# Performance work log

Measured on AMD Instinct MI355X. Metric: run time of the kernel, lower is better.

The kernel has to match this reference:

```python
import jax, jax.numpy as jnp
import numpy as np
from jax import lax

RES = 32          # feature map side, HW = RES*RES = 1024
HEADS = 32
QKD = 16          # sampled_qkdim
VD = 32           # sampled_vdim
L = HEADS * VD    # 1024, v channels

def _relative_position_index(res):
    # faithful to attn_pos_idx in the torch code
    coords = np.stack(np.meshgrid(np.arange(res), np.arange(res), indexing='ij'))  # [2,res,res]
    flat = coords.reshape(2, -1)
    rel = flat[:, :, None] - flat[:, None, :]        # [2, N, N]
    rel = rel.transpose(1, 2, 0).copy()
    rel[:, :, 0] += res - 1
    rel[:, :, 1] += res - 1
    rel[:, :, 0] *= 2 * res - 1
    return rel.sum(-1)                               # [N, N] int

_RPI = jnp.asarray(_relative_position_index(RES))    # [1024,1024]

def _hardswish(x):
    return x * jnp.clip(x + 3.0, 0.0, 6.0) * (1.0 / 6.0)

def setup_inputs() -> dict:
    key = jax.random.key(0)
    ks = jax.random.split(key, 6)
    B, HW, C = 4, RES * RES, 512
    x = jax.random.normal(ks[0], (B, HW, C), jnp.float32)
    w_qkv = jax.random.normal(ks[1], (2 * C + L, C), jnp.float32) * 0.02   # [2048,512]
    dw_kernel = jax.random.normal(ks[2], (L, 1, 3, 3), jnp.float32) * 0.1  # depthwise OIHW
    attn_bias = jax.random.normal(ks[3], ((2 * RES - 1) ** 2, HEADS), jnp.float32) * 0.02
    proj_w = jax.random.normal(ks[4], (C, L), jnp.float32) * 0.02
    proj_b = jax.random.normal(ks[5], (C,), jnp.float32) * 0.02
    return {"x": x, "w_qkv": w_qkv, "dw_kernel": dw_kernel,
            "attn_bias": attn_bias, "proj_w": proj_w, "proj_b": proj_b}

def reference(x, w_qkv, dw_kernel, attn_bias, proj_w, proj_b):
    B, HW, C = x.shape
    # elastic QKV projection (full sampled config == full weight)
    qkv = jnp.einsum('bnc,oc->bno', x, w_qkv)                    # [B,HW,2048]
    qkv = qkv.reshape(B, HW, HEADS, QKD + QKD + VD)
    q, k, v = jnp.split(qkv, [QKD, 2 * QKD], axis=3)             # per-head split
    q = q.transpose(0, 2, 1, 3)                                  # [B,H,HW,qkd]
    k = k.transpose(0, 2, 1, 3)
    # depthwise 3x3 conv on V path
    vimg = v.reshape(B, HW, L).transpose(0, 2, 1).reshape(B, L, RES, RES)
    vimg = lax.conv_general_dilated(vimg, dw_kernel, (1, 1), 'SAME',
                                    feature_group_count=L,
                                    dimension_numbers=('NCHW', 'OIHW', 'NCHW'))
    v = vimg.reshape(B, L, HW).transpose(0, 2, 1).reshape(B, HW, HEADS, VD)
    v = v.transpose(0, 2, 1, 3)                                  # [B,H,HW,vd]
    # attention with relative position bias
    attn = jnp.einsum('bhqd,bhkd->bhqk', q, k) * (QKD ** -0.5)   # [B,H,HW,HW]
    bias = attn_bias[_RPI.reshape(-1)].reshape(HW, HW, HEADS)
    bias = bias.transpose(2, 0, 1)[None]                         # [1,H,HW,HW]
    attn = jax.nn.softmax(attn + bias, axis=-1)
    out = jnp.einsum('bhqk,bhkd->bhqd', attn, v)
    out = out.transpose(0, 2, 1, 3).reshape(B, HW, L)
    out = _hardswish(out)
    out = jnp.einsum('bnl,cl->bnc', out, proj_w) + proj_b
    return out
```

## Files before the change

### kernel.cpp

```cpp
#include <hip/hip_runtime.h>
#include <stdint.h>

#define HEADS 32
#define HW_N 1024
#define QS 0.36067376022224085f
#define LOG2E 1.4426950408889634f

typedef __attribute__((ext_vector_type(8))) __bf16 bf16x8;
typedef __attribute__((ext_vector_type(4))) float f32x4;
typedef __attribute__((ext_vector_type(16))) float f32x16;
typedef __attribute__((ext_vector_type(4))) uint32_t u32x4;

__device__ __forceinline__ float b2f(uint16_t u) {
  union { uint32_t i; float f; } v; v.i = ((uint32_t)u) << 16; return v.f;
}
__device__ __forceinline__ uint16_t f2b(float f) {
  uint32_t u = __builtin_bit_cast(uint32_t, f);
  return (uint16_t)((u + 0x7FFFu + ((u >> 16) & 1u)) >> 16);
}

#define GLD16(g, s) __builtin_amdgcn_global_load_lds( \
    (const __attribute__((address_space(1))) void*)(g), \
    (__attribute__((address_space(3))) void*)(s), 16, 0, 0)

__global__ __launch_bounds__(256) void prep(const float* __restrict__ x,
                                            const float* __restrict__ wqv,
                                            const float* __restrict__ pw,
                                            const float* __restrict__ abias,
                                            uint16_t* __restrict__ xb,
                                            uint16_t* __restrict__ wqb,
                                            uint16_t* __restrict__ pwb,
                                            uint16_t* __restrict__ bt2b) {
  const int blk = blockIdx.x;
  const int tid = threadIdx.x;
  if (blk < 3584) {
    const float* in; uint16_t* out; int i;
    if (blk < 2048)      { in = x;   out = xb;  i = blk * 256 + tid; }
    else if (blk < 3072) { in = wqv; out = wqb; i = (blk - 2048) * 256 + tid; }
    else                 { in = pw;  out = pwb; i = (blk - 3072) * 256 + tid; }
    float4 v = ((const float4*)in)[i];
    ushort4 o;
    o.x = f2b(v.x); o.y = f2b(v.y); o.z = f2b(v.z); o.w = f2b(v.w);
    ((ushort4*)out)[i] = o;
  } else {
    const int blk2 = blk - 3584;
    const int h = blk2 / 63, d31 = blk2 - h * 63;
    const size_t tb = ((size_t)(h * 63 + d31)) << 10;
#pragma unroll
    for (int c = 0; c < 4; ++c) {
      const int idx = c * 256 + tid;
      const int lane = idx >> 4, r = idx & 15;
      const int hi = lane >> 5, ln = lane & 31;
      const int crow = (r & 3) + 8 * (r >> 2) + 4 * hi;
      const int col = 31 + ln - crow;
      bt2b[tb + idx] = f2b(LOG2E * abias[(size_t)(d31 * 63 + col) * 32 + h]);
    }
  }
}

__global__ __launch_bounds__(256) void gemm_qkv(
    const uint16_t* __restrict__ Aop, const uint16_t* __restrict__ Bop,
    uint16_t* __restrict__ qT, uint16_t* __restrict__ ko, uint16_t* __restrict__ vo) {
  const int K = 512;
  __shared__ uint16_t As[2][128 * 32];
  __shared__ uint16_t Bs[2][128 * 32];
  const int tid = threadIdx.x;
  const int lane = tid & 63;
  const int wave = tid >> 6;
  const int am0 = blockIdx.y * 128;
  const int bn0 = blockIdx.x * 128;
  const int m_off = (wave >> 1) * 64;
  const int n_off = (wave & 1) * 64;
  const int sr = tid >> 2;
  const int sc = (tid & 3) << 3;

  auto stage = [&](int buf, int kt) {
    const int k0 = kt << 5;
    GLD16(Aop + (size_t)(am0 + sr) * K + (k0 + sc), &As[buf][tid * 8]);
    GLD16(Aop + (size_t)(am0 + sr + 64) * K + (k0 + sc), &As[buf][(tid + 256) * 8]);
    GLD16(Bop + (size_t)(bn0 + sr) * K + (k0 + sc), &Bs[buf][tid * 8]);
    GLD16(Bop + (size_t)(bn0 + sr + 64) * K + (k0 + sc), &Bs[buf][(tid + 256) * 8]);
  };

  f32x4 acc[4][4] = {};
  stage(0, 0);
  asm volatile("s_waitcnt vmcnt(0)" ::: "memory");
  __syncthreads();

  const int fr = lane & 15;
  const int fk = (lane >> 4) << 3;
  int cur = 0;
  for (int kt = 0; kt < 16; ++kt) {
    if (kt + 1 < 16) stage(cur ^ 1, kt + 1);
    bf16x8 af[4], bf_[4];
#pragma unroll
    for (int mi = 0; mi < 4; ++mi)
      af[mi] = *(const bf16x8*)&As[cur][(m_off + mi * 16 + fr) * 32 + fk];
#pragma unroll
    for (int ni = 0; ni < 4; ++ni)
      bf_[ni] = *(const bf16x8*)&Bs[cur][(n_off + ni * 16 + fr) * 32 + fk];
#pragma unroll
    for (int mi = 0; mi < 4; ++mi)
#pragma unroll
      for (int ni = 0; ni < 4; ++ni)
        acc[mi][ni] = __builtin_amdgcn_mfma_f32_16x16x32_bf16(af[mi], bf_[ni], acc[mi][ni], 0, 0, 0);
    asm volatile("s_waitcnt vmcnt(0)" ::: "memory");
    __syncthreads();
    cur ^= 1;
  }

  const int rb = (lane >> 4) << 2;
  const int cl = lane & 15;
  const int b = am0 >> 10;
  const int h = (bn0 + n_off) >> 6;
  const int bh = b * 32 + h;
#pragma unroll
  for (int mi = 0; mi < 4; ++mi) {
    const int n0 = (am0 & 1023) + m_off + mi * 16 + rb;
    {
      ushort4 o;
      o.x = f2b(acc[mi][0][0] * QS); o.y = f2b(acc[mi][0][1] * QS);
      o.z = f2b(acc[mi][0][2] * QS); o.w = f2b(acc[mi][0][3] * QS);
      *(ushort4*)&qT[((size_t)(bh * 16 + cl) << 10) + n0] = o;
    }
#pragma unroll
    for (int r = 0; r < 4; ++r)
      ko[((size_t)(bh * 1024 + n0 + r)) * 16 + cl] = f2b(acc[mi][1][r]);
#pragma unroll
    for (int nv = 2; nv < 4; ++nv) {
      const int l = h * 32 + (nv - 2) * 16 + cl;
      ushort4 o;
      o.x = f2b(acc[mi][nv][0]); o.y = f2b(acc[mi][nv][1]);
      o.z = f2b(acc[mi][nv][2]); o.w = f2b(acc[mi][nv][3]);
      *(ushort4*)&vo[((size_t)(b * 1024 + l) << 10) + n0] = o;
    }
  }
}

__global__ __launch_bounds__(256) void dwconv3x3(const uint16_t* __restrict__ vimg,
                                                 const float* __restrict__ kw,
                                                 uint16_t* __restrict__ vcv) {
  __shared__ float t[1024];
  const int bl = blockIdx.x;
  const int l = bl & 1023;
  const int tid = threadIdx.x;
  const uint16_t* src = vimg + (size_t)bl * 1024;
  {
    uint2 vv = ((const uint2*)src)[tid];
    t[tid * 4 + 0] = b2f((uint16_t)vv.x);
    t[tid * 4 + 1] = b2f((uint16_t)(vv.x >> 16));
    t[tid * 4 + 2] = b2f((uint16_t)vv.y);
    t[tid * 4 + 3] = b2f((uint16_t)(vv.y >> 16));
  }
  float w[9];
#pragma unroll
  for (int i = 0; i < 9; ++i) w[i] = kw[l * 9 + i];
  __syncthreads();
  uint16_t* dst = vcv + (size_t)bl * 1024;
#pragma unroll
  for (int i = 0; i < 4; ++i) {
    const int p = tid + i * 256;
    const int y = p >> 5, x = p & 31;
    float a = 0.f;
#pragma unroll
    for (int dy = 0; dy < 3; ++dy) {
      const int yy = y + dy - 1;
      if (yy < 0 || yy > 31) continue;
#pragma unroll
      for (int dx = 0; dx < 3; ++dx) {
        const int xx = x + dx - 1;
        if (xx < 0 || xx > 31) continue;
        a += t[yy * 32 + xx] * w[dy * 3 + dx];
      }
    }
    dst[p] = f2b(a);
  }
}

__global__ __launch_bounds__(256, 4) void attn_mfma(
    const uint16_t* __restrict__ qT, const uint16_t* __restrict__ kb,
    const uint16_t* __restrict__ vt, const uint16_t* __restrict__ bt2b,
    uint16_t* __restrict__ hsO) {
  __shared__ __align__(16) uint16_t Ks[2][2][512];
  __shared__ __align__(16) uint16_t Vs[2][2][1024];
  __shared__ __align__(16) uint16_t Bs[7 * 1024];
  __shared__ float inv_s[128];
  const int blk = blockIdx.x;
  const int bh = blk & 127;
  const int qtg = blk >> 7;
  const int b = bh >> 5, h = bh & 31;
  const int tid = threadIdx.x;
  const int wave = tid >> 6, lane = tid & 63;
  const int hi = lane >> 5, ln = lane & 31;

  const int q0 = qtg * 128 + wave * 32;
  const int qi0 = qtg * 4;
  const int qi = qi0 + wave;

  union { ushort u[8]; bf16x8 v; } qu;
#pragma unroll
  for (int j = 0; j < 8; ++j)
    qu.u[j] = qT[((size_t)(bh * 16 + hi * 8 + j) << 10) + q0 + ln];
  const bf16x8 qf = qu.v;

  auto stageKV = [&](int buf, int t2) {
    if (tid < 128) {
      const int tile = tid >> 6, j = tid & 63;
      GLD16(kb + ((size_t)bh * 1024 + (t2 + tile) * 32 + (j & 31)) * 16 + ((j >> 5) & 1) * 8,
            &Ks[buf][tile][j * 8]);
    }
    {
      const int tile = tid >> 7, j = tid & 127;
      GLD16(vt + (((size_t)b * 1024 + h * 32 + (j & 31)) << 10) + (t2 + tile) * 32 + ((j >> 5) & 1) * 8 + ((j >> 6) & 1) * 16,
            &Vs[buf][tile][j * 8]);
    }
  };
  auto stageB = [&](int d31, int half) {
    if ((tid >> 7) == half) {
      const int j = tid & 127;
      GLD16(bt2b + (((size_t)h * 63 + d31) << 10) + (j & 63) * 16 + ((j >> 6) & 1) * 8,
            &Bs[(d31 % 7) * 1024 + j * 8]);
    }
  };

  stageKV(0, 0);
  stageB(qi0 + 30, 0); stageB(qi0 + 31, 1);
  stageB(qi0 + 32, 0); stageB(qi0 + 33, 1);
  stageB(qi0 + 34, 0);
  __syncthreads();

  f32x16 oacc = {};
  float ls0 = 0.f, ls1 = 0.f;
  int cur = 0;
  int slotA = (qi + 31) % 7;

#define COMPUTE(kf, ca, cb, vf0, vf1) do {                            \
    f32x16 cc;                                                        \
    _Pragma("unroll")                                                 \
    for (int j = 0; j < 4; ++j) {                                     \
      const uint32_t ua = ca[j], ub = cb[j];                          \
      cc[2 * j]     = __builtin_bit_cast(float, ua << 16);            \
      cc[2 * j + 1] = __builtin_bit_cast(float, ua & 0xFFFF0000u);    \
      cc[8 + 2 * j]     = __builtin_bit_cast(float, ub << 16);        \
      cc[8 + 2 * j + 1] = __builtin_bit_cast(float, ub & 0xFFFF0000u);\
    }                                                                 \
    const f32x16 s = __builtin_amdgcn_mfma_f32_32x32x16_bf16(kf, qf, cc, 0, 0, 0); \
    float p[16];                                                      \
    _Pragma("unroll")                                                 \
    for (int r = 0; r < 16; ++r) p[r] = __builtin_amdgcn_exp2f(s[r]); \
    _Pragma("unroll")                                                 \
    for (int r = 0; r < 8; ++r) { ls0 += p[r]; ls1 += p[r + 8]; }     \
    uint32_t w0, w1, w2, w3, w4, w5, w6, w7;                          \
    w0 = __builtin_amdgcn_perm(__builtin_bit_cast(uint32_t, p[1]),  __builtin_bit_cast(uint32_t, p[0]),  0x07060302u); \
    w1 = __builtin_amdgcn_perm(__builtin_bit_cast(uint32_t, p[3]),  __builtin_bit_cast(uint32_t, p[2]),  0x07060302u); \
    w2 = __builtin_amdgcn_perm(__builtin_bit_cast(uint32_t, p[5]),  __builtin_bit_cast(uint32_t, p[4]),  0x07060302u); \
    w3 = __builtin_amdgcn_perm(__builtin_bit_cast(uint32_t, p[7]),  __builtin_bit_cast(uint32_t, p[6]),  0x07060302u); \
    w4 = __builtin_amdgcn_perm(__builtin_bit_cast(uint32_t, p[9]),  __builtin_bit_cast(uint32_t, p[8]),  0x07060302u); \
    w5 = __builtin_amdgcn_perm(__builtin_bit_cast(uint32_t, p[11]), __builtin_bit_cast(uint32_t, p[10]), 0x07060302u); \
    w6 = __builtin_amdgcn_perm(__builtin_bit_cast(uint32_t, p[13]), __builtin_bit_cast(uint32_t, p[12]), 0x07060302u); \
    w7 = __builtin_amdgcn_perm(__builtin_bit_cast(uint32_t, p[15]), __builtin_bit_cast(uint32_t, p[14]), 0x07060302u); \
    asm("v_permlane32_swap_b32 %0, %1" : "+v"(w0), "+v"(w2));         \
    asm("v_permlane32_swap_b32 %0, %1" : "+v"(w1), "+v"(w3));         \
    asm("v_permlane32_swap_b32 %0, %1" : "+v"(w4), "+v"(w6));         \
    asm("v_permlane32_swap_b32 %0, %1" : "+v"(w5), "+v"(w7));         \
    const u32x4 a0u = {w0, w1, w2, w3};                               \
    const u32x4 a1u = {w4, w5, w6, w7};                               \
    oacc = __builtin_amdgcn_mfma_f32_32x32x16_bf16(                   \
        __builtin_bit_cast(bf16x8, a0u), vf0, oacc, 0, 0, 0);         \
    oacc = __builtin_amdgcn_mfma_f32_32x32x16_bf16(                   \
        __builtin_bit_cast(bf16x8, a1u), vf1, oacc, 0, 0, 0);         \
  } while (0)

  for (int s = 0; s < 16; ++s) {
    if (s < 15) {
      stageKV(cur ^ 1, 2 * s + 2);
      stageB(qi0 + 29 - 2 * s, 0);
      stageB(qi0 + 28 - 2 * s, 1);
    }
    const int slotB = slotA ? slotA - 1 : 6;
    {
      const bf16x8 kf  = *(const bf16x8*)&Ks[cur][0][lane * 8];
      const bf16x8 vf0 = *(const bf16x8*)&Vs[cur][0][lane * 8];
      const bf16x8 vf1 = *(const bf16x8*)&Vs[cur][0][512 + lane * 8];
      const u32x4 ca = *(const u32x4*)&Bs[slotA * 1024 + lane * 8];
      const u32x4 cb = *(const u32x4*)&Bs[slotA * 1024 + 512 + lane * 8];
      COMPUTE(kf, ca, cb, vf0, vf1);
    }
    {
      const bf16x8 kf  = *(const bf16x8*)&Ks[cur][1][lane * 8];
      const bf16x8 vf0 = *(const bf16x8*)&Vs[cur][1][lane * 8];
      const bf16x8 vf1 = *(const bf16x8*)&Vs[cur][1][512 + lane * 8];
      const u32x4 ca = *(const u32x4*)&Bs[slotB * 1024 + lane * 8];
      const u32x4 cb = *(const u32x4*)&Bs[slotB * 1024 + 512 + lane * 8];
      COMPUTE(kf, ca, cb, vf0, vf1);
    }
    __syncthreads();
    cur ^= 1;
    slotA = (slotA >= 2) ? slotA - 2 : slotA + 5;
  }
#undef COMPUTE

  const float lsum = ls0 + ls1;
  const float tot = lsum + __shfl_xor(lsum, 32);
  if (hi == 0) inv_s[wave * 32 + ln] = __builtin_amdgcn_rcpf(tot);
  const int ROWS[16] = {0,1,2,3,8,9,10,11,16,17,18,19,24,25,26,27};
#pragma unroll
  for (int r = 0; r < 16; ++r) {
    const int row = ROWS[r] + 4 * hi;
    const float o = oacc[r] * inv_s[wave * 32 + row];
    const float hs = o * fminf(fmaxf(o + 3.f, 0.f), 6.f) * (1.f / 6.f);
    hsO[((size_t)(b * 1024 + q0 + row) << 10) + h * 32 + ln] = f2b(hs);
  }
}

__global__ __launch_bounds__(256) void gemm_proj(
    const uint16_t* __restrict__ Aop, const uint16_t* __restrict__ Bop,
    float* __restrict__ Cout, const float* __restrict__ bias) {
  const int K = 1024;
  __shared__ uint16_t As[2][64 * 32];
  __shared__ uint16_t Bs[2][64 * 32];
  const int tid = threadIdx.x;
  const int lane = tid & 63;
  const int wave = tid >> 6;
  const int am0 = blockIdx.y * 64;
  const int bn0 = blockIdx.x * 64;
  const int m_off = (wave >> 1) * 32;
  const int n_off = (wave & 1) * 32;
  const int sr = tid >> 2;
  const int sc = (tid & 3) << 3;

  auto stage = [&](int buf, int kt) {
    const int k0 = kt << 5;
    GLD16(Aop + (size_t)(am0 + sr) * K + (k0 + sc), &As[buf][tid * 8]);
    GLD16(Bop + (size_t)(bn0 + sr) * K + (k0 + sc), &Bs[buf][tid * 8]);
  };

  f32x4 acc[2][2] = {};
  stage(0, 0);
  asm volatile("s_waitcnt vmcnt(0)" ::: "memory");
  __syncthreads();

  const int fr = lane & 15;
  const int fk = (lane >> 4) << 3;
  int cur = 0;
  for (int kt = 0; kt < 32; ++kt) {
    if (kt + 1 < 32) stage(cur ^ 1, kt + 1);
    bf16x8 af[2], bf_[2];
#pragma unroll
    for (int mi = 0; mi < 2; ++mi)
      af[mi] = *(const bf16x8*)&As[cur][(m_off + mi * 16 + fr) * 32 + fk];
#pragma unroll
    for (int ni = 0; ni < 2; ++ni)
      bf_[ni] = *(const bf16x8*)&Bs[cur][(n_off + ni * 16 + fr) * 32 + fk];
#pragma unroll
    for (int mi = 0; mi < 2; ++mi)
#pragma unroll
      for (int ni = 0; ni < 2; ++ni)
        acc[mi][ni] = __builtin_amdgcn_mfma_f32_16x16x32_bf16(af[mi], bf_[ni], acc[mi][ni], 0, 0, 0);
    asm volatile("s_waitcnt vmcnt(0)" ::: "memory");
    __syncthreads();
    cur ^= 1;
  }

  const int rb = (lane >> 4) << 2;
  const int cl = lane & 15;
#pragma unroll
  for (int mi = 0; mi < 2; ++mi)
#pragma unroll
    for (int ni = 0; ni < 2; ++ni) {
      const int cg = bn0 + n_off + ni * 16 + cl;
#pragma unroll
      for (int r = 0; r < 4; ++r) {
        const int rg = am0 + m_off + mi * 16 + rb + r;
        Cout[(size_t)rg * 512 + cg] = acc[mi][ni][r] + bias[cg];
      }
    }
}

extern "C" void kernel_launch(void* const* d_in, const int* in_sizes, int n_in,
                              void* d_out, int out_size, void* d_ws, size_t ws_size,
                              hipStream_t stream) {
  const float* x      = (const float*)d_in[0];
  const float* w_qkv  = (const float*)d_in[1];
  const float* dwk    = (const float*)d_in[2];
  const float* abias  = (const float*)d_in[3];
  const float* pw     = (const float*)d_in[4];
  const float* pb     = (const float*)d_in[5];
  float* out = (float*)d_out;

  char* ws = (char*)d_ws;
  uint16_t* xb   = (uint16_t*)(ws);
  uint16_t* wqb  = (uint16_t*)(ws + (4ull << 20));
  uint16_t* pwb  = (uint16_t*)(ws + (6ull << 20));
  uint16_t* qT   = (uint16_t*)(ws + (7ull << 20));
  uint16_t* kbuf = (uint16_t*)(ws + (11ull << 20));
  uint16_t* vimg = (uint16_t*)(ws + (15ull << 20));
  uint16_t* vcv  = (uint16_t*)(ws + (23ull << 20));
  uint16_t* bt2b = (uint16_t*)(ws + (31ull << 20));
  uint16_t* hsO  = vimg;

  prep<<<5600, 256, 0, stream>>>(x, w_qkv, pw, abias, xb, wqb, pwb, bt2b);
  gemm_qkv<<<dim3(16, 32), 256, 0, stream>>>(xb, wqb, qT, kbuf, vimg);
  dwconv3x3<<<4096, 256, 0, stream>>>(vimg, dwk, vcv);
  attn_mfma<<<1024, 256, 0, stream>>>(qT, kbuf, vcv, bt2b, hsO);
  gemm_proj<<<dim3(8, 64), 256, 0, stream>>>(hsO, pwb, out, pb);
}
```

Before: 85.15 us.

## Halve QKV GEMM N-tile, stage bias row in LDS, raise attention MFMA priority

The QKV GEMM now uses 128x64 tiles, one head per block, so it launches twice as many blocks (1024 instead of 512) for better CU occupancy. Each wave pair handles either the q/k columns or the v columns, and the epilogue branches on that. The bias-table prep loads the 63 needed bias values into shared memory once per block instead of doing a gathered global read per element. The attention inner loop wraps its MFMA section in s_setprio to favour compute waves. The cost is more redundant A-tile loads in the GEMM and an added barrier in prep.

```diff
diff --git a/kernel.cpp b/kernel.cpp
--- a/kernel.cpp
+++ b/kernel.cpp
@@ -43,8 +43,11 @@
     o.x = f2b(v.x); o.y = f2b(v.y); o.z = f2b(v.z); o.w = f2b(v.w);
     ((ushort4*)out)[i] = o;
   } else {
+    __shared__ float rv[63];
     const int blk2 = blk - 3584;
     const int h = blk2 / 63, d31 = blk2 - h * 63;
+    if (tid < 63) rv[tid] = LOG2E * abias[(size_t)(d31 * 63 + tid) * 32 + h];
+    __syncthreads();
     const size_t tb = ((size_t)(h * 63 + d31)) << 10;
 #pragma unroll
     for (int c = 0; c < 4; ++c) {
@@ -53,7 +56,7 @@
       const int hi = lane >> 5, ln = lane & 31;
       const int crow = (r & 3) + 8 * (r >> 2) + 4 * hi;
       const int col = 31 + ln - crow;
-      bt2b[tb + idx] = f2b(LOG2E * abias[(size_t)(d31 * 63 + col) * 32 + h]);
+      bt2b[tb + idx] = f2b(rv[col]);
     }
   }
 }
@@ -63,26 +66,23 @@
     uint16_t* __restrict__ qT, uint16_t* __restrict__ ko, uint16_t* __restrict__ vo) {
   const int K = 512;
   __shared__ uint16_t As[2][128 * 32];
-  __shared__ uint16_t Bs[2][128 * 32];
+  __shared__ uint16_t Bs[2][64 * 32];
   const int tid = threadIdx.x;
   const int lane = tid & 63;
   const int wave = tid >> 6;
   const int am0 = blockIdx.y * 128;
-  const int bn0 = blockIdx.x * 128;
-  const int m_off = (wave >> 1) * 64;
-  const int n_off = (wave & 1) * 64;
-  const int sr = tid >> 2;
+  const int bn0 = blockIdx.x * 64;
+  const int wr = wave >> 1, wc = wave & 1;
   const int sc = (tid & 3) << 3;
 
   auto stage = [&](int buf, int kt) {
     const int k0 = kt << 5;
-    GLD16(Aop + (size_t)(am0 + sr) * K + (k0 + sc), &As[buf][tid * 8]);
-    GLD16(Aop + (size_t)(am0 + sr + 64) * K + (k0 + sc), &As[buf][(tid + 256) * 8]);
-    GLD16(Bop + (size_t)(bn0 + sr) * K + (k0 + sc), &Bs[buf][tid * 8]);
-    GLD16(Bop + (size_t)(bn0 + sr + 64) * K + (k0 + sc), &Bs[buf][(tid + 256) * 8]);
+    GLD16(Aop + (size_t)(am0 + (tid >> 2)) * K + (k0 + sc), &As[buf][tid * 8]);
+    GLD16(Aop + (size_t)(am0 + 64 + (tid >> 2)) * K + (k0 + sc), &As[buf][(tid + 256) * 8]);
+    GLD16(Bop + (size_t)(bn0 + (tid >> 2)) * K + (k0 + sc), &Bs[buf][tid * 8]);
   };
 
-  f32x4 acc[4][4] = {};
+  f32x4 acc[4][2] = {};
   stage(0, 0);
   asm volatile("s_waitcnt vmcnt(0)" ::: "memory");
   __syncthreads();
@@ -92,17 +92,17 @@
   int cur = 0;
   for (int kt = 0; kt < 16; ++kt) {
     if (kt + 1 < 16) stage(cur ^ 1, kt + 1);
-    bf16x8 af[4], bf_[4];
+    bf16x8 af[4], bf_[2];
 #pragma unroll
     for (int mi = 0; mi < 4; ++mi)
-      af[mi] = *(const bf16x8*)&As[cur][(m_off + mi * 16 + fr) * 32 + fk];
-#pragma unroll
-    for (int ni = 0; ni < 4; ++ni)
-      bf_[ni] = *(const bf16x8*)&Bs[cur][(n_off + ni * 16 + fr) * 32 + fk];
+      af[mi] = *(const bf16x8*)&As[cur][(wr * 64 + mi * 16 + fr) * 32 + fk];
+#pragma unroll
+    for (int ni = 0; ni < 2; ++ni)
+      bf_[ni] = *(const bf16x8*)&Bs[cur][(wc * 32 + ni * 16 + fr) * 32 + fk];
 #pragma unroll
     for (int mi = 0; mi < 4; ++mi)
 #pragma unroll
-      for (int ni = 0; ni < 4; ++ni)
+      for (int ni = 0; ni < 2; ++ni)
         acc[mi][ni] = __builtin_amdgcn_mfma_f32_16x16x32_bf16(af[mi], bf_[ni], acc[mi][ni], 0, 0, 0);
     asm volatile("s_waitcnt vmcnt(0)" ::: "memory");
     __syncthreads();
@@ -112,27 +112,30 @@
   const int rb = (lane >> 4) << 2;
   const int cl = lane & 15;
   const int b = am0 >> 10;
-  const int h = (bn0 + n_off) >> 6;
+  const int h = blockIdx.x;
   const int bh = b * 32 + h;
 #pragma unroll
   for (int mi = 0; mi < 4; ++mi) {
-    const int n0 = (am0 & 1023) + m_off + mi * 16 + rb;
-    {
-      ushort4 o;
-      o.x = f2b(acc[mi][0][0] * QS); o.y = f2b(acc[mi][0][1] * QS);
-      o.z = f2b(acc[mi][0][2] * QS); o.w = f2b(acc[mi][0][3] * QS);
-      *(ushort4*)&qT[((size_t)(bh * 16 + cl) << 10) + n0] = o;
-    }
-#pragma unroll
-    for (int r = 0; r < 4; ++r)
-      ko[((size_t)(bh * 1024 + n0 + r)) * 16 + cl] = f2b(acc[mi][1][r]);
-#pragma unroll
-    for (int nv = 2; nv < 4; ++nv) {
-      const int l = h * 32 + (nv - 2) * 16 + cl;
-      ushort4 o;
-      o.x = f2b(acc[mi][nv][0]); o.y = f2b(acc[mi][nv][1]);
-      o.z = f2b(acc[mi][nv][2]); o.w = f2b(acc[mi][nv][3]);
-      *(ushort4*)&vo[((size_t)(b * 1024 + l) << 10) + n0] = o;
+    const int n0 = (am0 & 1023) + wr * 64 + mi * 16 + rb;
+    if (wc == 0) {
+      {
+        ushort4 o;
+        o.x = f2b(acc[mi][0][0] * QS); o.y = f2b(acc[mi][0][1] * QS);
+        o.z = f2b(acc[mi][0][2] * QS); o.w = f2b(acc[mi][0][3] * QS);
+        *(ushort4*)&qT[((size_t)(bh * 16 + cl) << 10) + n0] = o;
+      }
+#pragma unroll
+      for (int r = 0; r < 4; ++r)
+        ko[((size_t)(bh * 1024 + n0 + r)) * 16 + cl] = f2b(acc[mi][1][r]);
+    } else {
+#pragma unroll
+      for (int ni = 0; ni < 2; ++ni) {
+        const int l = h * 32 + ni * 16 + cl;
+        ushort4 o;
+        o.x = f2b(acc[mi][ni][0]); o.y = f2b(acc[mi][ni][1]);
+        o.z = f2b(acc[mi][ni][2]); o.w = f2b(acc[mi][ni][3]);
+        *(ushort4*)&vo[((size_t)(b * 1024 + l) << 10) + n0] = o;
+      }
     }
   }
 }
@@ -278,6 +281,7 @@
       stageB(qi0 + 28 - 2 * s, 1);
     }
     const int slotB = slotA ? slotA - 1 : 6;
+    __builtin_amdgcn_s_setprio(1);
     {
       const bf16x8 kf  = *(const bf16x8*)&Ks[cur][0][lane * 8];
       const bf16x8 vf0 = *(const bf16x8*)&Vs[cur][0][lane * 8];
@@ -294,6 +298,7 @@
       const u32x4 cb = *(const u32x4*)&Bs[slotB * 1024 + 512 + lane * 8];
       COMPUTE(kf, ca, cb, vf0, vf1);
     }
+    __builtin_amdgcn_s_setprio(0);
     __syncthreads();
     cur ^= 1;
     slotA = (slotA >= 2) ? slotA - 2 : slotA + 5;
@@ -400,7 +405,7 @@
   uint16_t* hsO  = vimg;
 
   prep<<<5600, 256, 0, stream>>>(x, w_qkv, pw, abias, xb, wqb, pwb, bt2b);
-  gemm_qkv<<<dim3(16, 32), 256, 0, stream>>>(xb, wqb, qT, kbuf, vimg);
+  gemm_qkv<<<dim3(32, 32), 256, 0, stream>>>(xb, wqb, qT, kbuf, vimg);
   dwconv3x3<<<4096, 256, 0, stream>>>(vimg, dwk, vcv);
   attn_mfma<<<1024, 256, 0, stream>>>(qT, kbuf, vcv, bt2b, hsO);
   gemm_proj<<<dim3(8, 64), 256, 0, stream>>>(hsO, pwb, out, pb);
```

After: 84.38 us. No clear change (-0.9%).
